# Kernel tuning notes

Hardware: AMD Instinct MI355X
Metric: run time of the kernel (lower is better)

## Reference

```python
import jax, jax.numpy as jnp
import numpy as np

N_NODES = 50000
N_EDGES = 1600000


def gcn_conv(x, edge_index, W, b, n):
    # PyG GCNConv: linear (no bias), add self-loops, symmetric deg^{-1/2} norm,
    # scatter-add aggregation to dst, then bias.
    src, dst = edge_index[0], edge_index[1]
    loops = jnp.arange(n, dtype=src.dtype)
    src = jnp.concatenate([src, loops])
    dst = jnp.concatenate([dst, loops])
    h = x @ W  # [N, out]
    deg = jax.ops.segment_sum(jnp.ones(dst.shape, dtype=h.dtype), dst, num_segments=n)
    dinv = jax.lax.rsqrt(jnp.maximum(deg, 1.0))  # deg >= 1 due to self-loops
    norm = dinv[src] * dinv[dst]  # [E+N]
    msg = h[src] * norm[:, None]  # gather + scale
    out = jax.ops.segment_sum(msg, dst, num_segments=n)  # scatter-add
    return out + b


def setup_inputs() -> dict:
    key = jax.random.key(0)
    ks = jax.random.split(key, 8)
    x = jax.random.normal(ks[0], (N_NODES, 256), dtype=jnp.float32)
    edge_index = jax.random.randint(ks[1], (2, N_EDGES), 0, N_NODES, dtype=jnp.int64)
    s = 0.05
    W1 = jax.random.normal(ks[2], (256, 256), dtype=jnp.float32) * s
    b1 = jax.random.normal(ks[3], (256,), dtype=jnp.float32) * s
    W2 = jax.random.normal(ks[4], (256, 128), dtype=jnp.float32) * s
    b2 = jax.random.normal(ks[5], (128,), dtype=jnp.float32) * s
    Wl = jax.random.normal(ks[6], (128, 64), dtype=jnp.float32) * s
    bl = jax.random.normal(ks[7], (64,), dtype=jnp.float32) * s
    return {"x": x, "edge_index": edge_index, "W1": W1, "b1": b1,
            "W2": W2, "b2": b2, "Wl": Wl, "bl": bl}


def reference(x, edge_index, W1, b1, W2, b2, Wl, bl):
    n = x.shape[0]
    h = jax.nn.relu(gcn_conv(x, edge_index, W1, b1, n))
    h = jax.nn.relu(gcn_conv(h, edge_index, W2, b2, n))
    return h @ Wl + bl
```

## Files before the change

### kernel.cpp

```cpp
#include <hip/hip_runtime.h>
#include <hip/hip_bf16.h>
#include <cstdint>
#include <cstddef>


using frag_ab = __attribute__((ext_vector_type(8))) short;
using f32x4   = __attribute__((ext_vector_type(4))) float;
typedef unsigned short u16;

#define NB 1024

__device__ __forceinline__ short f2bf(float f) {
    return __builtin_bit_cast(short, __float2bfloat16(f));
}


__global__ __launch_bounds__(256) void count_kernel(const int* __restrict__ dst, int E,
                                                    int* __restrict__ counts) {
    int i = blockIdx.x * blockDim.x + threadIdx.x;
    int stride = gridDim.x * blockDim.x;
    for (; i < E; i += stride) atomicAdd(&counts[dst[i]], 1);
}

__global__ __launch_bounds__(256) void dinv_kernel(const int* __restrict__ counts,
                                                   float* __restrict__ dinv, int n) {
    int i = blockIdx.x * blockDim.x + threadIdx.x;
    if (i < n) dinv[i] = rsqrtf((float)(counts[i] + 1));
}

__global__ __launch_bounds__(1024) void scan_kernel(const int* __restrict__ counts,
                                                    int* __restrict__ offs,
                                                    int n, int total) {
    __shared__ int ssum[1024];
    const int tid = threadIdx.x;
    const int chunk = (n + 1023) / 1024;
    const int beg = tid * chunk;
    const int end = min(beg + chunk, n);
    int local = 0;
    for (int i = beg; i < end; ++i) local += counts[i];
    ssum[tid] = local;
    __syncthreads();
    for (int off = 1; off < 1024; off <<= 1) {
        int v = (tid >= off) ? ssum[tid - off] : 0;
        __syncthreads();
        ssum[tid] += v;
        __syncthreads();
    }
    int run = ssum[tid] - local;
    for (int i = beg; i < end; ++i) {
        offs[i] = run;
        run += counts[i];
    }
    if (tid == 0) offs[n] = total;
}


template<int PASS>
__global__ __launch_bounds__(256) void hist_kernel(const void* __restrict__ in,
                                                   int E, int CH,
                                                   int* __restrict__ h) {
    __shared__ int hist[256];
    const int b = blockIdx.x;
    const int t = threadIdx.x;
    hist[t] = 0;
    __syncthreads();
    const int beg = b * CH;
    const int end = min(beg + CH, E);
    if constexpr (PASS == 1) {
        const int* dst = (const int*)in;
        for (int i = beg + t; i < end; i += 256) atomicAdd(&hist[dst[i] & 255], 1);
    } else {
        const uint2* rec = (const uint2*)in;
        for (int i = beg + t; i < end; i += 256) atomicAdd(&hist[(int)(rec[i].x >> 8)], 1);
    }
    __syncthreads();
    h[t * NB + b] = hist[t];
}

__global__ __launch_bounds__(256) void row_scan_kernel(int* __restrict__ h,
                                                       int* __restrict__ tot) {
    __shared__ int part[256];
    const int d = blockIdx.x;
    const int t = threadIdx.x;
    int* row = h + (size_t)d * NB;
    int4 v = *(int4*)(row + t * 4);
    const int s = v.x + v.y + v.z + v.w;
    part[t] = s;
    __syncthreads();
    for (int o = 1; o < 256; o <<= 1) {
        int u = (t >= o) ? part[t - o] : 0;
        __syncthreads();
        part[t] += u;
        __syncthreads();
    }
    const int ex = part[t] - s;
    int4 o4;
    o4.x = ex;
    o4.y = ex + v.x;
    o4.z = ex + v.x + v.y;
    o4.w = ex + v.x + v.y + v.z;
    *(int4*)(row + t * 4) = o4;
    if (t == 255) tot[d] = part[255];
}

__global__ __launch_bounds__(256) void digit_scan_kernel(const int* __restrict__ tot,
                                                         int* __restrict__ digbase) {
    __shared__ int s[256];
    const int t = threadIdx.x;
    const int v = tot[t];
    s[t] = v;
    __syncthreads();
    for (int o = 1; o < 256; o <<= 1) {
        int u = (t >= o) ? s[t - o] : 0;
        __syncthreads();
        s[t] += u;
        __syncthreads();
    }
    digbase[t] = s[t] - v;
}

template<int PASS>
__global__ __launch_bounds__(64) void scatter_kernel(const void* __restrict__ in,
                                                     const int* __restrict__ srcv,
                                                     int E, int CH,
                                                     const int* __restrict__ base,
                                                     const int* __restrict__ digbase,
                                                     void* __restrict__ outv) {
    __shared__ int cur[256];
    const int b = blockIdx.x;
    const int lane = threadIdx.x;
    for (int t = lane; t < 256; t += 64) cur[t] = base[t * NB + b] + digbase[t];
    const int beg = b * CH;
    const int end = min(beg + CH, E);
    const unsigned long long below = (1ull << lane) - 1;
    for (int i0 = beg; i0 < end; i0 += 64) {
        const int i = i0 + lane;
        const bool act = i < end;
        int d = 0, s = 0;
        if (act) {
            if constexpr (PASS == 1) {
                d = ((const int*)in)[i];
                s = srcv[i];
            } else {
                uint2 r = ((const uint2*)in)[i];
                d = (int)r.x;
                s = (int)r.y;
            }
        }
        const int dig = (PASS == 1) ? (d & 255) : (d >> 8);
        unsigned long long m = __ballot(act);
#pragma unroll
        for (int bit = 0; bit < 8; ++bit) {
            unsigned long long bb = __ballot((dig >> bit) & 1);
            m &= ((dig >> bit) & 1) ? bb : ~bb;
        }
        if (act) {
            const int rank = __popcll(m & below);
            const int cnt = __popcll(m);
            const int c = cur[dig];
            if (rank == cnt - 1) cur[dig] = c + cnt;
            if constexpr (PASS == 1)
                ((uint2*)outv)[c + rank] = make_uint2((unsigned)d, (unsigned)s);
            else
                ((int*)outv)[c + rank] = s;
        }
    }
}


__global__ __launch_bounds__(256) void prep_w(const float* __restrict__ W,
                                              short* __restrict__ Wt, int K, int N) {
    int i = blockIdx.x * 256 + threadIdx.x;
    if (i >= K * N) return;
    int k = i / N, nn = i - k * N;
    Wt[(size_t)nn * K + k] = f2bf(W[i]);
}

template<int WM, int WN, int NI, bool A_BF16, bool SCALE, bool BIAS, bool OUT_BF16>
__global__ __launch_bounds__(256) void gemm_mfma(const void* __restrict__ Av,
                                                 const short* __restrict__ Bt,
                                                 const float* __restrict__ dinv,
                                                 const float* __restrict__ bias,
                                                 void* __restrict__ Cv,
                                                 int M, int N, int K) {
    constexpr int TM = WM * 64;
    constexpr int TN = WN * NI * 16;
    const int wid = threadIdx.x >> 6;
    const int lane = threadIdx.x & 63;
    const int wm = wid / WN;
    const int wn = wid % WN;
    const int bm = blockIdx.y * TM + wm * 64;
    const int bn = blockIdx.x * TN + wn * NI * 16;
    const int r15 = lane & 15;
    const int g = lane >> 4;

    f32x4 acc[4][NI] = {};

    int arow[4];
#pragma unroll
    for (int mi = 0; mi < 4; ++mi) arow[mi] = min(bm + mi * 16 + r15, M - 1);

    for (int k0 = 0; k0 < K; k0 += 32) {
        const int kb = k0 + g * 8;
        frag_ab af[4];
#pragma unroll
        for (int mi = 0; mi < 4; ++mi) {
            if constexpr (A_BF16) {
                af[mi] = *(const frag_ab*)((const short*)Av + (size_t)arow[mi] * K + kb);
            } else {
                const float* ap = (const float*)Av + (size_t)arow[mi] * K + kb;
                float4 lo = *(const float4*)ap;
                float4 hi = *(const float4*)(ap + 4);
                frag_ab t;
                t[0] = f2bf(lo.x); t[1] = f2bf(lo.y); t[2] = f2bf(lo.z); t[3] = f2bf(lo.w);
                t[4] = f2bf(hi.x); t[5] = f2bf(hi.y); t[6] = f2bf(hi.z); t[7] = f2bf(hi.w);
                af[mi] = t;
            }
        }
        frag_ab bf[NI];
#pragma unroll
        for (int ni = 0; ni < NI; ++ni)
            bf[ni] = *(const frag_ab*)(Bt + (size_t)(bn + ni * 16 + r15) * K + kb);
#pragma unroll
        for (int mi = 0; mi < 4; ++mi)
#pragma unroll
            for (int ni = 0; ni < NI; ++ni)
                acc[mi][ni] = __builtin_amdgcn_mfma_f32_16x16x32_bf16(af[mi], bf[ni],
                                                                      acc[mi][ni], 0, 0, 0);
    }

#pragma unroll
    for (int mi = 0; mi < 4; ++mi) {
#pragma unroll
        for (int j = 0; j < 4; ++j) {
            const int row = bm + mi * 16 + g * 4 + j;
            if (row >= M) continue;
            const float s = SCALE ? dinv[row] : 1.0f;
#pragma unroll
            for (int ni = 0; ni < NI; ++ni) {
                const int col = bn + ni * 16 + r15;
                float v = acc[mi][ni][j] * s;
                if (BIAS) v += bias[col];
                if constexpr (OUT_BF16)
                    ((short*)Cv)[(size_t)row * N + col] = f2bf(v);
                else
                    ((float*)Cv)[(size_t)row * N + col] = v;
            }
        }
    }
}

template<int V>
__device__ __forceinline__ void vloadbf(float (&d)[V], const u16* __restrict__ p) {
    if constexpr (V == 4) {
        uint2 u = *(const uint2*)p;
        d[0] = __builtin_bit_cast(float, u.x << 16);
        d[1] = __builtin_bit_cast(float, u.x & 0xffff0000u);
        d[2] = __builtin_bit_cast(float, u.y << 16);
        d[3] = __builtin_bit_cast(float, u.y & 0xffff0000u);
    } else {
        unsigned u = *(const unsigned*)p;
        d[0] = __builtin_bit_cast(float, u << 16);
        d[1] = __builtin_bit_cast(float, u & 0xffff0000u);
    }
}

template<int V>
__global__ __launch_bounds__(256) void agg_kernel(const u16* __restrict__ hs,
                                                  const int* __restrict__ csr,
                                                  const int* __restrict__ offs,
                                                  const float* __restrict__ dinv,
                                                  const float* __restrict__ bias,
                                                  u16* __restrict__ out,
                                                  int n, int F) {
    const int node = blockIdx.x * 4 + (threadIdx.x >> 6);
    if (node >= n) return;
    const int lane = threadIdx.x & 63;
    const int c0 = lane * V;

    float self[V];
    vloadbf<V>(self, hs + (size_t)node * F + c0);

    float acc[V];
#pragma unroll
    for (int j = 0; j < V; ++j) acc[j] = 0.f;

    int e = offs[node];
    const int end = offs[node + 1];
    for (; e + 4 <= end; e += 4) {
        int s0 = csr[e], s1 = csr[e + 1], s2 = csr[e + 2], s3 = csr[e + 3];
        float t0[V], t1[V], t2[V], t3[V];
        vloadbf<V>(t0, hs + (size_t)s0 * F + c0);
        vloadbf<V>(t1, hs + (size_t)s1 * F + c0);
        vloadbf<V>(t2, hs + (size_t)s2 * F + c0);
        vloadbf<V>(t3, hs + (size_t)s3 * F + c0);
#pragma unroll
        for (int j = 0; j < V; ++j) acc[j] += ((t0[j] + t1[j]) + (t2[j] + t3[j]));
    }
    for (; e < end; ++e) {
        float tv[V];
        vloadbf<V>(tv, hs + (size_t)csr[e] * F + c0);
#pragma unroll
        for (int j = 0; j < V; ++j) acc[j] += tv[j];
    }

    const float di = dinv[node];
    u16 res[V];
#pragma unroll
    for (int j = 0; j < V; ++j) {
        float v = fmaf(acc[j] + self[j], di, bias[c0 + j]);
        res[j] = (u16)f2bf(fmaxf(v, 0.f));
    }
    if constexpr (V == 4) {
        uint2 o;
        o.x = (unsigned)res[0] | ((unsigned)res[1] << 16);
        o.y = (unsigned)res[2] | ((unsigned)res[3] << 16);
        *(uint2*)(out + (size_t)node * F + c0) = o;
    } else {
        unsigned o = (unsigned)res[0] | ((unsigned)res[1] << 16);
        *(unsigned*)(out + (size_t)node * F + c0) = o;
    }
}


extern "C" void kernel_launch(void* const* d_in, const int* in_sizes, int n_in,
                              void* d_out, int out_size, void* d_ws, size_t ws_size,
                              hipStream_t stream) {
    const float* x  = (const float*)d_in[0];
    const int*   ei = (const int*)d_in[1];
    const float* W1 = (const float*)d_in[2];
    const float* b1 = (const float*)d_in[3];
    const float* W2 = (const float*)d_in[4];
    const float* b2 = (const float*)d_in[5];
    const float* Wl = (const float*)d_in[6];
    const float* bl = (const float*)d_in[7];

    const int E = in_sizes[1] / 2;
    const int n = in_sizes[0] / 256;
    const int* src = ei;
    const int* dst = ei + E;
    const int CH = (E + NB - 1) / NB;

    char* ws = (char*)d_ws;
    size_t off = 0;
    auto alloc = [&](size_t bytes) -> void* {
        void* p = ws + off;
        off += (bytes + 255) & ~(size_t)255;
        return p;
    };
    short* h      = (short*)alloc((size_t)n * 256 * 2);
    short* a      = (short*)alloc((size_t)n * 256 * 2);
    int*   counts = (int*)alloc((size_t)n * 4);
    int*   offs   = (int*)alloc((size_t)(n + 1) * 4);
    float* dinv   = (float*)alloc((size_t)n * 4);
    int*   csr    = (int*)alloc((size_t)E * 4);
    int*   h1     = (int*)alloc((size_t)NB * 256 * 4);
    int*   h2     = (int*)alloc((size_t)NB * 256 * 4);
    int*   tot1   = (int*)alloc(256 * 4);
    int*   tot2   = (int*)alloc(256 * 4);
    int*   db1    = (int*)alloc(256 * 4);
    int*   db2    = (int*)alloc(256 * 4);
    short* wt1    = (short*)alloc((size_t)256 * 256 * 2);
    short* wt2    = (short*)alloc((size_t)128 * 256 * 2);
    short* wtl    = (short*)alloc((size_t)64 * 128 * 2);
    uint2* rec1   = (uint2*)a;
    (void)ws_size;

    hipMemsetAsync(counts, 0, (size_t)n * 4, stream);
    prep_w<<<(256 * 256 + 255) / 256, 256, 0, stream>>>(W1, wt1, 256, 256);
    prep_w<<<(256 * 128 + 255) / 256, 256, 0, stream>>>(W2, wt2, 256, 128);
    prep_w<<<(128 * 64 + 255) / 256, 256, 0, stream>>>(Wl, wtl, 128, 64);

    count_kernel<<<1024, 256, 0, stream>>>(dst, E, counts);
    dinv_kernel<<<(n + 255) / 256, 256, 0, stream>>>(counts, dinv, n);
    scan_kernel<<<1, 1024, 0, stream>>>(counts, offs, n, E);

    hist_kernel<1><<<NB, 256, 0, stream>>>(dst, E, CH, h1);
    row_scan_kernel<<<256, 256, 0, stream>>>(h1, tot1);
    digit_scan_kernel<<<1, 256, 0, stream>>>(tot1, db1);
    scatter_kernel<1><<<NB, 64, 0, stream>>>(dst, src, E, CH, h1, db1, rec1);
    hist_kernel<2><<<NB, 256, 0, stream>>>(rec1, E, CH, h2);
    row_scan_kernel<<<256, 256, 0, stream>>>(h2, tot2);
    digit_scan_kernel<<<1, 256, 0, stream>>>(tot2, db2);
    scatter_kernel<2><<<NB, 64, 0, stream>>>(rec1, nullptr, E, CH, h2, db2, csr);

    gemm_mfma<2, 2, 4, false, true, false, true>
        <<<dim3(2, (n + 127) / 128), 256, 0, stream>>>(x, wt1, dinv, nullptr, h, n, 256, 256);
    agg_kernel<4><<<(n + 3) / 4, 256, 0, stream>>>((const u16*)h, csr, offs, dinv, b1,
                                                   (u16*)a, n, 256);

    gemm_mfma<1, 4, 2, true, true, false, true>
        <<<dim3(1, (n + 63) / 64), 256, 0, stream>>>(a, wt2, dinv, nullptr, h, n, 128, 256);
    agg_kernel<2><<<(n + 3) / 4, 256, 0, stream>>>((const u16*)h, csr, offs, dinv, b2,
                                                   (u16*)a, n, 128);

    gemm_mfma<1, 4, 1, true, false, true, false>
        <<<dim3(1, (n + 63) / 64), 256, 0, stream>>>(a, wtl, nullptr, bl, d_out, n, 64, 128);
}
```

Baseline: 571.8 us.

## Slice aggregation by 64-byte feature chunks and fold dinv into scan

Replaces the per-node aggregation kernel with a feature-sliced variant. Each 16-lane group handles one node's 32-column slice, and the 8 blocks in a group of consecutive block indices cover different slices of the same node range, with the aim of improving L2 locality of gathered rows and giving more parallel memory requests per byte. It also removes the separate dinv kernel by computing rsqrt inside the serial scan loop, which saves a launch but adds work to the single-block scan. Each gather is now a 4-byte load covering 2 columns, so more, smaller memory transactions are issued.

```diff
diff --git a/kernel.cpp b/kernel.cpp
--- a/kernel.cpp
+++ b/kernel.cpp
@@ -22,14 +22,9 @@
     for (; i < E; i += stride) atomicAdd(&counts[dst[i]], 1);
 }
 
-__global__ __launch_bounds__(256) void dinv_kernel(const int* __restrict__ counts,
-                                                   float* __restrict__ dinv, int n) {
-    int i = blockIdx.x * blockDim.x + threadIdx.x;
-    if (i < n) dinv[i] = rsqrtf((float)(counts[i] + 1));
-}
-
 __global__ __launch_bounds__(1024) void scan_kernel(const int* __restrict__ counts,
                                                     int* __restrict__ offs,
+                                                    float* __restrict__ dinv,
                                                     int n, int total) {
     __shared__ int ssum[1024];
     const int tid = threadIdx.x;
@@ -37,7 +32,11 @@
     const int beg = tid * chunk;
     const int end = min(beg + chunk, n);
     int local = 0;
-    for (int i = beg; i < end; ++i) local += counts[i];
+    for (int i = beg; i < end; ++i) {
+        const int c = counts[i];
+        dinv[i] = rsqrtf((float)(c + 1));
+        local += c;
+    }
     ssum[tid] = local;
     __syncthreads();
     for (int off = 1; off < 1024; off <<= 1) {
@@ -250,76 +249,61 @@
     }
 }
 
-template<int V>
-__device__ __forceinline__ void vloadbf(float (&d)[V], const u16* __restrict__ p) {
-    if constexpr (V == 4) {
-        uint2 u = *(const uint2*)p;
-        d[0] = __builtin_bit_cast(float, u.x << 16);
-        d[1] = __builtin_bit_cast(float, u.x & 0xffff0000u);
-        d[2] = __builtin_bit_cast(float, u.y << 16);
-        d[3] = __builtin_bit_cast(float, u.y & 0xffff0000u);
-    } else {
-        unsigned u = *(const unsigned*)p;
-        d[0] = __builtin_bit_cast(float, u << 16);
-        d[1] = __builtin_bit_cast(float, u & 0xffff0000u);
-    }
-}
-
-template<int V>
-__global__ __launch_bounds__(256) void agg_kernel(const u16* __restrict__ hs,
+template<int NSL>
+__global__ __launch_bounds__(256) void agg_sliced(const u16* __restrict__ hs,
                                                   const int* __restrict__ csr,
                                                   const int* __restrict__ offs,
                                                   const float* __restrict__ dinv,
                                                   const float* __restrict__ bias,
-                                                  u16* __restrict__ out,
-                                                  int n, int F) {
-    const int node = blockIdx.x * 4 + (threadIdx.x >> 6);
+                                                  u16* __restrict__ out, int n) {
+    constexpr int F = NSL * 32;
+    constexpr int DUP = 8 / NSL;
+    const int bsl = blockIdx.x & 7;
+    const int slice = bsl & (NSL - 1);
+    const int node = (blockIdx.x >> 3) * (16 * DUP) + (bsl / NSL) * 16
+                   + (threadIdx.x >> 4);
     if (node >= n) return;
-    const int lane = threadIdx.x & 63;
-    const int c0 = lane * V;
-
-    float self[V];
-    vloadbf<V>(self, hs + (size_t)node * F + c0);
-
-    float acc[V];
-#pragma unroll
-    for (int j = 0; j < V; ++j) acc[j] = 0.f;
-
+    const int r = threadIdx.x & 15;
+    const int c0 = slice * 32 + r * 2;
+    const u16* hb = hs + c0;
+
+#define LD2(row, A, B)                                                   \
+    {                                                                    \
+        unsigned u = *(const unsigned*)(hb + (size_t)(row) * F);         \
+        A = __builtin_bit_cast(float, u << 16);                          \
+        B = __builtin_bit_cast(float, u & 0xffff0000u);                  \
+    }
+
+    float s0, s1;
+    LD2(node, s0, s1);
+
+    float a0 = 0.f, a1 = 0.f;
     int e = offs[node];
     const int end = offs[node + 1];
     for (; e + 4 <= end; e += 4) {
-        int s0 = csr[e], s1 = csr[e + 1], s2 = csr[e + 2], s3 = csr[e + 3];
-        float t0[V], t1[V], t2[V], t3[V];
-        vloadbf<V>(t0, hs + (size_t)s0 * F + c0);
-        vloadbf<V>(t1, hs + (size_t)s1 * F + c0);
-        vloadbf<V>(t2, hs + (size_t)s2 * F + c0);
-        vloadbf<V>(t3, hs + (size_t)s3 * F + c0);
-#pragma unroll
-        for (int j = 0; j < V; ++j) acc[j] += ((t0[j] + t1[j]) + (t2[j] + t3[j]));
+        int i0 = csr[e], i1 = csr[e + 1], i2 = csr[e + 2], i3 = csr[e + 3];
+        float t00, t01, t10, t11, t20, t21, t30, t31;
+        LD2(i0, t00, t01);
+        LD2(i1, t10, t11);
+        LD2(i2, t20, t21);
+        LD2(i3, t30, t31);
+        a0 += ((t00 + t10) + (t20 + t30));
+        a1 += ((t01 + t11) + (t21 + t31));
     }
     for (; e < end; ++e) {
-        float tv[V];
-        vloadbf<V>(tv, hs + (size_t)csr[e] * F + c0);
-#pragma unroll
-        for (int j = 0; j < V; ++j) acc[j] += tv[j];
-    }
+        float t0, t1;
+        LD2(csr[e], t0, t1);
+        a0 += t0;
+        a1 += t1;
+    }
+#undef LD2
 
     const float di = dinv[node];
-    u16 res[V];
-#pragma unroll
-    for (int j = 0; j < V; ++j) {
-        float v = fmaf(acc[j] + self[j], di, bias[c0 + j]);
-        res[j] = (u16)f2bf(fmaxf(v, 0.f));
-    }
-    if constexpr (V == 4) {
-        uint2 o;
-        o.x = (unsigned)res[0] | ((unsigned)res[1] << 16);
-        o.y = (unsigned)res[2] | ((unsigned)res[3] << 16);
-        *(uint2*)(out + (size_t)node * F + c0) = o;
-    } else {
-        unsigned o = (unsigned)res[0] | ((unsigned)res[1] << 16);
-        *(unsigned*)(out + (size_t)node * F + c0) = o;
-    }
+    float v0 = fmaf(a0 + s0, di, bias[c0]);
+    float v1 = fmaf(a1 + s1, di, bias[c0 + 1]);
+    unsigned o = (unsigned)(u16)f2bf(fmaxf(v0, 0.f)) |
+                 ((unsigned)(u16)f2bf(fmaxf(v1, 0.f)) << 16);
+    *(unsigned*)(out + (size_t)node * F + c0) = o;
 }
 
 
@@ -372,8 +356,7 @@
     prep_w<<<(128 * 64 + 255) / 256, 256, 0, stream>>>(Wl, wtl, 128, 64);
 
     count_kernel<<<1024, 256, 0, stream>>>(dst, E, counts);
-    dinv_kernel<<<(n + 255) / 256, 256, 0, stream>>>(counts, dinv, n);
-    scan_kernel<<<1, 1024, 0, stream>>>(counts, offs, n, E);
+    scan_kernel<<<1, 1024, 0, stream>>>(counts, offs, dinv, n, E);
 
     hist_kernel<1><<<NB, 256, 0, stream>>>(dst, E, CH, h1);
     row_scan_kernel<<<256, 256, 0, stream>>>(h1, tot1);
@@ -386,13 +369,13 @@
 
     gemm_mfma<2, 2, 4, false, true, false, true>
         <<<dim3(2, (n + 127) / 128), 256, 0, stream>>>(x, wt1, dinv, nullptr, h, n, 256, 256);
-    agg_kernel<4><<<(n + 3) / 4, 256, 0, stream>>>((const u16*)h, csr, offs, dinv, b1,
-                                                   (u16*)a, n, 256);
+    agg_sliced<8><<<8 * ((n + 15) / 16), 256, 0, stream>>>((const u16*)h, csr, offs,
+                                                           dinv, b1, (u16*)a, n);
 
     gemm_mfma<1, 4, 2, true, true, false, true>
         <<<dim3(1, (n + 63) / 64), 256, 0, stream>>>(a, wt2, dinv, nullptr, h, n, 128, 256);
-    agg_kernel<2><<<(n + 3) / 4, 256, 0, stream>>>((const u16*)h, csr, offs, dinv, b2,
-                                                   (u16*)a, n, 128);
+    agg_sliced<4><<<8 * ((n + 31) / 32), 256, 0, stream>>>((const u16*)h, csr, offs,
+                                                           dinv, b2, (u16*)a, n);
 
     gemm_mfma<1, 4, 1, true, false, true, false>
         <<<dim3(1, (n + 63) / 64), 256, 0, stream>>>(a, wtl, nullptr, bl, d_out, n, 64, 128);
```

Result: slower. 684.2 us (+19.7%).
